# Kernel optimization log

Measured on AMD Instinct MI355X. Metric: run time of the kernel, lower is better.

The kernel has to match this reference:

```python
import jax, jax.numpy as jnp
import numpy as np

D_MODEL = 1024

def setup_inputs() -> dict:
    key = jax.random.key(0)
    kx, kq, kk, kv, ko = jax.random.split(key, 5)
    B, S, D = 8, 2048, D_MODEL
    scale = 1.0 / np.sqrt(D)
    x = jax.random.normal(kx, (B, S, D), dtype=jnp.float32)
    # nn.Linear weights are [out, in]; y = x @ W.T
    Wq = jax.random.normal(kq, (D, D), dtype=jnp.float32) * scale
    Wk = jax.random.normal(kk, (D, D), dtype=jnp.float32) * scale
    Wv = jax.random.normal(kv, (D, D), dtype=jnp.float32) * scale
    Wo = jax.random.normal(ko, (D, D), dtype=jnp.float32) * scale
    return {"x": x, "Wq": Wq, "Wk": Wk, "Wv": Wv, "Wo": Wo}

def reference(x, Wq, Wk, Wv, Wo):
    # Single-head self-attention, dropout in eval mode (identity).
    d_model = x.shape[-1]
    q = jnp.einsum('bsd,ed->bse', x, Wq)
    k = jnp.einsum('bsd,ed->bse', x, Wk)
    v = jnp.einsum('bsd,ed->bse', x, Wv)
    scores = jnp.einsum('bqe,bke->bqk', q, k) / jnp.sqrt(jnp.float32(d_model))
    attn = jax.nn.softmax(scores, axis=-1)
    weighted = jnp.einsum('bqk,bke->bqe', attn, v)
    return jnp.einsum('bqe,oe->bqo', weighted, Wo)
```

## Files before the change

### kernel.cpp

```cpp
#include <hip/hip_runtime.h>
#include <hip/hip_bf16.h>
#include <stdint.h>

typedef short bf16x8 __attribute__((ext_vector_type(8)));
typedef float f32x4 __attribute__((ext_vector_type(4)));

__device__ __forceinline__ unsigned short f2bf(float x) {
  uint32_t u = __builtin_bit_cast(uint32_t, x);
  u += 0x7FFFu + ((u >> 16) & 1u);
  return (unsigned short)(u >> 16);
}
__device__ __forceinline__ float bf2f(unsigned short u) {
  uint32_t v = ((uint32_t)u) << 16;
  return __builtin_bit_cast(float, v);
}

__device__ __forceinline__ void gl2lds16(const void* g, void* l) {
  __builtin_amdgcn_global_load_lds(
      (const __attribute__((address_space(1))) unsigned int*)g,
      (__attribute__((address_space(3))) unsigned int*)l, 16, 0, 0);
}

__global__ __launch_bounds__(256) void cast_f32_bf16_k(
    const float* __restrict__ s, unsigned short* __restrict__ d, long n) {
  long i = ((long)blockIdx.x * 256 + threadIdx.x) * 8;
  if (i >= n) return;
  float4 a = *(const float4*)(s + i);
  float4 b = *(const float4*)(s + i + 4);
  bf16x8 o;
  o[0] = (short)f2bf(a.x); o[1] = (short)f2bf(a.y);
  o[2] = (short)f2bf(a.z); o[3] = (short)f2bf(a.w);
  o[4] = (short)f2bf(b.x); o[5] = (short)f2bf(b.y);
  o[6] = (short)f2bf(b.z); o[7] = (short)f2bf(b.w);
  *(bf16x8*)(d + i) = o;
}

__global__ __launch_bounds__(256) void cast4_f32_bf16_k(
    const float* __restrict__ s0, const float* __restrict__ s1,
    const float* __restrict__ s2, const float* __restrict__ s3,
    unsigned short* __restrict__ d, long n) {
  const float* s = blockIdx.z == 0 ? s0 : blockIdx.z == 1 ? s1 : blockIdx.z == 2 ? s2 : s3;
  long i = ((long)blockIdx.x * 256 + threadIdx.x) * 8;
  if (i >= n) return;
  float4 a = *(const float4*)(s + i);
  float4 b = *(const float4*)(s + i + 4);
  bf16x8 o;
  o[0] = (short)f2bf(a.x); o[1] = (short)f2bf(a.y);
  o[2] = (short)f2bf(a.z); o[3] = (short)f2bf(a.w);
  o[4] = (short)f2bf(b.x); o[5] = (short)f2bf(b.y);
  o[6] = (short)f2bf(b.z); o[7] = (short)f2bf(b.w);
  *(bf16x8*)(d + blockIdx.z * n + i) = o;
}

template <typename OutT, bool FUSEQKV>
__global__ __launch_bounds__(512, 2) void gemm_bt8(
    const unsigned short* __restrict__ A, const unsigned short* __restrict__ B,
    OutT* __restrict__ C, int M, int N, int K,
    long sA, long sB, long sC, float alpha) {
  extern __shared__ __align__(16) char smem[];
  const int bz = blockIdx.z;
  const int gx = gridDim.x;
  const int nwg = gx * gridDim.y;
  const int idx = blockIdx.y * gx + blockIdx.x;
  const int wg = (idx & 7) * (nwg >> 3) + (idx >> 3);
  const int bm = wg / gx, bn = wg % gx;

  const int tid = threadIdx.x, lane = tid & 63, wave = tid >> 6;
  const int wm = wave >> 2, wn = wave & 3;

  const char* Ac = (const char*)(A + (long)bz * sA + (long)bm * 256 * K);
  const char* Bc = (const char*)(B + (long)bz * sB + (long)bn * 256 * K);
  C += (long)bz * sC;
  const long ld = (long)K * 2;

  const int sr8 = tid >> 3;
  const int scolx = (((tid & 7) ^ ((tid >> 3) & 7)) << 4);

  auto stageHalf = [&](int t, int op, int h, const char* gbase) {
    char* reg = smem + (((((t & 1) << 1) | op) << 1 | h) << 14);
    const long ktb = (long)t << 7;
#pragma unroll
    for (int c = 0; c < 2; ++c)
      gl2lds16(gbase + (long)(h * 128 + c * 64 + sr8) * ld + ktb + scolx,
               reg + c * 8192 + tid * 16);
  };

  const char* Areg[2] = { smem + ((0 << 2 | wm) << 14),
                          smem + ((1 << 2 | wm) << 14) };
  const char* Breg[2] = { smem + (((0 << 2) | 2 | (wn >> 1)) << 14),
                          smem + (((1 << 2) | 2 | (wn >> 1)) << 14) };
  const int cko[2] = { (((lane >> 4) << 4) ^ ((lane & 7) << 4)),
                       ((64 | ((lane >> 4) << 4)) ^ ((lane & 7) << 4)) };
  const int rowA0 = (lane & 15) * 128;
  const int rowB0 = ((wn & 1) * 64 + (lane & 15)) * 128;

  f32x4 acc[8][4] = {};

  stageHalf(0, 1, 0, Bc); stageHalf(0, 1, 1, Bc);
  stageHalf(0, 0, 0, Ac); stageHalf(0, 0, 1, Ac);
  stageHalf(1, 1, 0, Bc); stageHalf(1, 1, 1, Bc);
  asm volatile("s_waitcnt vmcnt(4)" ::: "memory");
  __builtin_amdgcn_s_barrier();

  const int nt = K >> 6;
  const int niter = nt >> 1;
  for (int i = 0; i < niter; ++i) {
    const int u = 2 * i;
    const bool pf = (i + 1 < niter);
#pragma unroll
    for (int d = 0; d < 2; ++d) {
      bf16x8 b[4][2];
#pragma unroll
      for (int mq = 0; mq < 4; ++mq) {
        bf16x8 a[2][2];
        if (mq == 0) {
#pragma unroll
          for (int n = 0; n < 4; ++n)
#pragma unroll
            for (int kh = 0; kh < 2; ++kh)
              b[n][kh] = *(const bf16x8*)(Breg[d] + rowB0 + n * 2048 + cko[kh]);
        }
#pragma unroll
        for (int j = 0; j < 2; ++j)
#pragma unroll
          for (int kh = 0; kh < 2; ++kh)
            a[j][kh] = *(const bf16x8*)(Areg[d] + rowA0 + (mq * 2 + j) * 2048 + cko[kh]);
        if (d == 0 && mq == 0) { stageHalf(u + 1, 0, 0, Ac); stageHalf(u + 1, 0, 1, Ac); }
        if (d == 0 && mq == 1 && pf) stageHalf(u + 2, 1, 0, Bc);
        if (d == 0 && mq == 2 && pf) stageHalf(u + 2, 1, 1, Bc);
        if (d == 1 && mq == 0 && pf) { stageHalf(u + 2, 0, 0, Ac); stageHalf(u + 2, 0, 1, Ac); }
        if (d == 1 && mq == 1 && pf) stageHalf(u + 3, 1, 0, Bc);
        if (d == 1 && mq == 2 && pf) stageHalf(u + 3, 1, 1, Bc);
        if (mq == 0) asm volatile("s_waitcnt lgkmcnt(8)" ::: "memory");
        __builtin_amdgcn_s_barrier();
        asm volatile("s_waitcnt lgkmcnt(0)" ::: "memory");
        __builtin_amdgcn_sched_barrier(0);
        __builtin_amdgcn_s_setprio(1);
#pragma unroll
        for (int kh = 0; kh < 2; ++kh)
#pragma unroll
          for (int j = 0; j < 2; ++j)
#pragma unroll
            for (int n = 0; n < 4; ++n)
              acc[mq * 2 + j][n] = __builtin_amdgcn_mfma_f32_16x16x32_bf16(
                  a[j][kh], b[n][kh], acc[mq * 2 + j][n], 0, 0, 0);
        __builtin_amdgcn_s_setprio(0);
        if (d == 0 && mq == 3) {
          if (pf) asm volatile("s_waitcnt vmcnt(4)" ::: "memory");
          else    asm volatile("s_waitcnt vmcnt(0)" ::: "memory");
        }
        if (d == 1 && mq == 3 && pf) asm volatile("s_waitcnt vmcnt(4)" ::: "memory");
        __builtin_amdgcn_s_barrier();
      }
    }
  }

  const long row0 = (long)bm * 256 + wm * 128 + (lane >> 4) * 4;
  const int col0 = bn * 256 + wn * 64 + (lane & 15);
  if constexpr (FUSEQKV) {
    const int tensor = bn >> 2;
    unsigned short* dst = (unsigned short*)C + ((long)tensor << 24);
    const int colb0 = col0 - (tensor << 10);
#pragma unroll
    for (int m = 0; m < 8; ++m) {
#pragma unroll
      for (int n = 0; n < 4; ++n) {
        if (tensor < 2) {
#pragma unroll
          for (int r = 0; r < 4; ++r)
            dst[(row0 + m * 16 + r) * 1024 + colb0 + n * 16] = f2bf(acc[m][n][r]);
        } else {
          long row = row0 + m * 16;
          long base = ((row >> 11) << 21) + ((long)(colb0 + n * 16) << 11) + (row & 2047);
          ushort4 st;
          st.x = f2bf(acc[m][n][0]); st.y = f2bf(acc[m][n][1]);
          st.z = f2bf(acc[m][n][2]); st.w = f2bf(acc[m][n][3]);
          *(ushort4*)(dst + base) = st;
        }
      }
    }
  } else {
#pragma unroll
    for (int m = 0; m < 8; ++m) {
#pragma unroll
      for (int n = 0; n < 4; ++n) {
#pragma unroll
        for (int r = 0; r < 4; ++r) {
          long row = row0 + m * 16 + r;
          int col = col0 + n * 16;
          float v = acc[m][n][r] * alpha;
          if constexpr (sizeof(OutT) == 2)
            C[row * (long)N + col] = (OutT)f2bf(v);
          else
            C[row * (long)N + col] = v;
        }
      }
    }
  }
}

__global__ __launch_bounds__(256) void softmax_inplace(unsigned short* __restrict__ s, int C) {
  __shared__ float red[8];
  long row = blockIdx.x;
  unsigned short* p = s + row * (long)C;
  int tid = threadIdx.x, lane = tid & 63, w = tid >> 6;
  bf16x8 raw = *(const bf16x8*)(p + tid * 8);
  float v[8];
  float mx = -3.4e38f;
#pragma unroll
  for (int j = 0; j < 8; ++j) { v[j] = bf2f((unsigned short)raw[j]); mx = fmaxf(mx, v[j]); }
#pragma unroll
  for (int o = 32; o > 0; o >>= 1) mx = fmaxf(mx, __shfl_xor(mx, o));
  if (lane == 0) red[w] = mx;
  __syncthreads();
  mx = fmaxf(fmaxf(red[0], red[1]), fmaxf(red[2], red[3]));
  float sum = 0.f;
#pragma unroll
  for (int j = 0; j < 8; ++j) { v[j] = __expf(v[j] - mx); sum += v[j]; }
#pragma unroll
  for (int o = 32; o > 0; o >>= 1) sum += __shfl_xor(sum, o);
  if (lane == 0) red[4 + w] = sum;
  __syncthreads();
  float inv = 1.f / (red[4] + red[5] + red[6] + red[7]);
  bf16x8 o8;
#pragma unroll
  for (int j = 0; j < 8; ++j) o8[j] = (short)f2bf(v[j] * inv);
  *(bf16x8*)(p + tid * 8) = o8;
}

extern "C" void kernel_launch(void* const* d_in, const int* in_sizes, int n_in,
                              void* d_out, int out_size, void* d_ws, size_t ws_size,
                              hipStream_t stream) {
  (void)in_sizes; (void)n_in; (void)out_size; (void)ws_size;
  const float* x  = (const float*)d_in[0];
  const float* Wq = (const float*)d_in[1];
  const float* Wk = (const float*)d_in[2];
  const float* Wv = (const float*)d_in[3];
  const float* Wo = (const float*)d_in[4];
  const int B = 8, S = 2048, D = 1024;
  const long MB = 1 << 20;
  char* w = (char*)d_ws;
  unsigned short* Wqb = (unsigned short*)(w + 0 * MB);
  unsigned short* Wob = (unsigned short*)(w + 6 * MB);
  unsigned short* xb  = (unsigned short*)(w + 8 * MB);
  unsigned short* qb  = (unsigned short*)(w + 40 * MB);
  unsigned short* kb  = (unsigned short*)(w + 72 * MB);
  unsigned short* vt  = (unsigned short*)(w + 104 * MB);
  unsigned short* wb  = xb;
  unsigned short* attn = (unsigned short*)d_out;
  float* out = (float*)d_out;

  long nx = (long)B * S * D;
  long nw = (long)D * D;

  const int LDSB = 131072;
  hipFuncSetAttribute((const void*)gemm_bt8<unsigned short, true>,
                      hipFuncAttributeMaxDynamicSharedMemorySize, LDSB);
  hipFuncSetAttribute((const void*)gemm_bt8<unsigned short, false>,
                      hipFuncAttributeMaxDynamicSharedMemorySize, LDSB);
  hipFuncSetAttribute((const void*)gemm_bt8<float, false>,
                      hipFuncAttributeMaxDynamicSharedMemorySize, LDSB);

  cast_f32_bf16_k<<<(int)(nx / 2048), 256, 0, stream>>>(x, xb, nx);
  dim3 gW((int)(nw / 2048), 1, 4);
  cast4_f32_bf16_k<<<gW, 256, 0, stream>>>(Wq, Wk, Wv, Wo, Wqb, nw);

  dim3 gF(3072 / 256, (B * S) / 256, 1);
  gemm_bt8<unsigned short, true><<<gF, 512, LDSB, stream>>>(
      xb, Wqb, qb, B * S, 3072, D, 0, 0, 0, 1.f);

  dim3 gS(S / 256, S / 256, B);
  gemm_bt8<unsigned short, false><<<gS, 512, LDSB, stream>>>(qb, kb, attn, S, S, D,
      (long)S * D, (long)S * D, (long)S * S, 0.03125f);

  softmax_inplace<<<B * S, 256, 0, stream>>>(attn, S);

  dim3 gPV(D / 256, S / 256, B);
  gemm_bt8<unsigned short, false><<<gPV, 512, LDSB, stream>>>(attn, vt, wb, S, D, S,
      (long)S * S, (long)D * S, (long)S * D, 1.f);

  dim3 gP(D / 256, (B * S) / 256, 1);
  gemm_bt8<float, false><<<gP, 512, LDSB, stream>>>(wb, Wob, out, B * S, D, D, 0, 0, 0, 1.f);
}
```

Before: 329.4 us.

## Swap GEMM operands so every epilogue writes transposed vectorized stores

The GEMM kernel is generalized with separate leading dimensions for A, B and the output, and it always writes the output transposed, packing four contiguous rows per store. Each matmul is re-expressed with its operands swapped, computing C^T = B·A^T, so the accumulator's four consecutive rows become contiguous in memory. The fused QKV launch is split into three separate GEMMs, and V is written directly in its transposed layout. The aim is to replace scalar 2-byte and 4-byte scattered epilogue stores with 8-byte and 16-byte vector stores, at the cost of losing the single fused QKV launch.

```diff
diff --git a/kernel.cpp b/kernel.cpp
--- a/kernel.cpp
+++ b/kernel.cpp
@@ -52,11 +52,11 @@
   *(bf16x8*)(d + blockIdx.z * n + i) = o;
 }
 
-template <typename OutT, bool FUSEQKV>
-__global__ __launch_bounds__(512, 2) void gemm_bt8(
+template <typename OutT>
+__global__ __launch_bounds__(512, 2) void gemm_tt(
     const unsigned short* __restrict__ A, const unsigned short* __restrict__ B,
-    OutT* __restrict__ C, int M, int N, int K,
-    long sA, long sB, long sC, float alpha) {
+    OutT* __restrict__ C, int K,
+    long sA, long sB, long sC, int ldA, int ldB, int ldT, float alpha) {
   extern __shared__ __align__(16) char smem[];
   const int bz = blockIdx.z;
   const int gx = gridDim.x;
@@ -68,20 +68,20 @@
   const int tid = threadIdx.x, lane = tid & 63, wave = tid >> 6;
   const int wm = wave >> 2, wn = wave & 3;
 
-  const char* Ac = (const char*)(A + (long)bz * sA + (long)bm * 256 * K);
-  const char* Bc = (const char*)(B + (long)bz * sB + (long)bn * 256 * K);
+  const long ldAb = (long)ldA * 2, ldBb = (long)ldB * 2;
+  const char* Ac = (const char*)(A + (long)bz * sA) + (long)bm * 256 * ldAb;
+  const char* Bc = (const char*)(B + (long)bz * sB) + (long)bn * 256 * ldBb;
   C += (long)bz * sC;
-  const long ld = (long)K * 2;
 
   const int sr8 = tid >> 3;
   const int scolx = (((tid & 7) ^ ((tid >> 3) & 7)) << 4);
 
-  auto stageHalf = [&](int t, int op, int h, const char* gbase) {
+  auto stageHalf = [&](int t, int op, int h, const char* gbase, long ldb_) {
     char* reg = smem + (((((t & 1) << 1) | op) << 1 | h) << 14);
     const long ktb = (long)t << 7;
 #pragma unroll
     for (int c = 0; c < 2; ++c)
-      gl2lds16(gbase + (long)(h * 128 + c * 64 + sr8) * ld + ktb + scolx,
+      gl2lds16(gbase + (long)(h * 128 + c * 64 + sr8) * ldb_ + ktb + scolx,
                reg + c * 8192 + tid * 16);
   };
 
@@ -96,9 +96,9 @@
 
   f32x4 acc[8][4] = {};
 
-  stageHalf(0, 1, 0, Bc); stageHalf(0, 1, 1, Bc);
-  stageHalf(0, 0, 0, Ac); stageHalf(0, 0, 1, Ac);
-  stageHalf(1, 1, 0, Bc); stageHalf(1, 1, 1, Bc);
+  stageHalf(0, 1, 0, Bc, ldBb); stageHalf(0, 1, 1, Bc, ldBb);
+  stageHalf(0, 0, 0, Ac, ldAb); stageHalf(0, 0, 1, Ac, ldAb);
+  stageHalf(1, 1, 0, Bc, ldBb); stageHalf(1, 1, 1, Bc, ldBb);
   asm volatile("s_waitcnt vmcnt(4)" ::: "memory");
   __builtin_amdgcn_s_barrier();
 
@@ -125,12 +125,12 @@
 #pragma unroll
           for (int kh = 0; kh < 2; ++kh)
             a[j][kh] = *(const bf16x8*)(Areg[d] + rowA0 + (mq * 2 + j) * 2048 + cko[kh]);
-        if (d == 0 && mq == 0) { stageHalf(u + 1, 0, 0, Ac); stageHalf(u + 1, 0, 1, Ac); }
-        if (d == 0 && mq == 1 && pf) stageHalf(u + 2, 1, 0, Bc);
-        if (d == 0 && mq == 2 && pf) stageHalf(u + 2, 1, 1, Bc);
-        if (d == 1 && mq == 0 && pf) { stageHalf(u + 2, 0, 0, Ac); stageHalf(u + 2, 0, 1, Ac); }
-        if (d == 1 && mq == 1 && pf) stageHalf(u + 3, 1, 0, Bc);
-        if (d == 1 && mq == 2 && pf) stageHalf(u + 3, 1, 1, Bc);
+        if (d == 0 && mq == 0) { stageHalf(u + 1, 0, 0, Ac, ldAb); stageHalf(u + 1, 0, 1, Ac, ldAb); }
+        if (d == 0 && mq == 1 && pf) stageHalf(u + 2, 1, 0, Bc, ldBb);
+        if (d == 0 && mq == 2 && pf) stageHalf(u + 2, 1, 1, Bc, ldBb);
+        if (d == 1 && mq == 0 && pf) { stageHalf(u + 2, 0, 0, Ac, ldAb); stageHalf(u + 2, 0, 1, Ac, ldAb); }
+        if (d == 1 && mq == 1 && pf) stageHalf(u + 3, 1, 0, Bc, ldBb);
+        if (d == 1 && mq == 2 && pf) stageHalf(u + 3, 1, 1, Bc, ldBb);
         if (mq == 0) asm volatile("s_waitcnt lgkmcnt(8)" ::: "memory");
         __builtin_amdgcn_s_barrier();
         asm volatile("s_waitcnt lgkmcnt(0)" ::: "memory");
@@ -157,43 +157,23 @@
 
   const long row0 = (long)bm * 256 + wm * 128 + (lane >> 4) * 4;
   const int col0 = bn * 256 + wn * 64 + (lane & 15);
-  if constexpr (FUSEQKV) {
-    const int tensor = bn >> 2;
-    unsigned short* dst = (unsigned short*)C + ((long)tensor << 24);
-    const int colb0 = col0 - (tensor << 10);
-#pragma unroll
-    for (int m = 0; m < 8; ++m) {
-#pragma unroll
-      for (int n = 0; n < 4; ++n) {
-        if (tensor < 2) {
-#pragma unroll
-          for (int r = 0; r < 4; ++r)
-            dst[(row0 + m * 16 + r) * 1024 + colb0 + n * 16] = f2bf(acc[m][n][r]);
-        } else {
-          long row = row0 + m * 16;
-          long base = ((row >> 11) << 21) + ((long)(colb0 + n * 16) << 11) + (row & 2047);
-          ushort4 st;
-          st.x = f2bf(acc[m][n][0]); st.y = f2bf(acc[m][n][1]);
-          st.z = f2bf(acc[m][n][2]); st.w = f2bf(acc[m][n][3]);
-          *(ushort4*)(dst + base) = st;
-        }
-      }
-    }
-  } else {
-#pragma unroll
-    for (int m = 0; m < 8; ++m) {
-#pragma unroll
-      for (int n = 0; n < 4; ++n) {
-#pragma unroll
-        for (int r = 0; r < 4; ++r) {
-          long row = row0 + m * 16 + r;
-          int col = col0 + n * 16;
-          float v = acc[m][n][r] * alpha;
-          if constexpr (sizeof(OutT) == 2)
-            C[row * (long)N + col] = (OutT)f2bf(v);
-          else
-            C[row * (long)N + col] = v;
-        }
+#pragma unroll
+  for (int m = 0; m < 8; ++m) {
+#pragma unroll
+    for (int n = 0; n < 4; ++n) {
+      long row = row0 + m * 16;
+      long col = col0 + n * 16;
+      long base = col * (long)ldT + row;
+      if constexpr (sizeof(OutT) == 2) {
+        ushort4 st;
+        st.x = f2bf(acc[m][n][0] * alpha); st.y = f2bf(acc[m][n][1] * alpha);
+        st.z = f2bf(acc[m][n][2] * alpha); st.w = f2bf(acc[m][n][3] * alpha);
+        *(ushort4*)((unsigned short*)C + base) = st;
+      } else {
+        float4 st;
+        st.x = acc[m][n][0] * alpha; st.y = acc[m][n][1] * alpha;
+        st.z = acc[m][n][2] * alpha; st.w = acc[m][n][3] * alpha;
+        *(float4*)((float*)C + base) = st;
       }
     }
   }
@@ -241,6 +221,8 @@
   const long MB = 1 << 20;
   char* w = (char*)d_ws;
   unsigned short* Wqb = (unsigned short*)(w + 0 * MB);
+  unsigned short* Wkb = (unsigned short*)(w + 2 * MB);
+  unsigned short* Wvb = (unsigned short*)(w + 4 * MB);
   unsigned short* Wob = (unsigned short*)(w + 6 * MB);
   unsigned short* xb  = (unsigned short*)(w + 8 * MB);
   unsigned short* qb  = (unsigned short*)(w + 40 * MB);
@@ -254,31 +236,35 @@
   long nw = (long)D * D;
 
   const int LDSB = 131072;
-  hipFuncSetAttribute((const void*)gemm_bt8<unsigned short, true>,
+  hipFuncSetAttribute((const void*)gemm_tt<unsigned short>,
                       hipFuncAttributeMaxDynamicSharedMemorySize, LDSB);
-  hipFuncSetAttribute((const void*)gemm_bt8<unsigned short, false>,
-                      hipFuncAttributeMaxDynamicSharedMemorySize, LDSB);
-  hipFuncSetAttribute((const void*)gemm_bt8<float, false>,
+  hipFuncSetAttribute((const void*)gemm_tt<float>,
                       hipFuncAttributeMaxDynamicSharedMemorySize, LDSB);
 
   cast_f32_bf16_k<<<(int)(nx / 2048), 256, 0, stream>>>(x, xb, nx);
   dim3 gW((int)(nw / 2048), 1, 4);
   cast4_f32_bf16_k<<<gW, 256, 0, stream>>>(Wq, Wk, Wv, Wo, Wqb, nw);
 
-  dim3 gF(3072 / 256, (B * S) / 256, 1);
-  gemm_bt8<unsigned short, true><<<gF, 512, LDSB, stream>>>(
-      xb, Wqb, qb, B * S, 3072, D, 0, 0, 0, 1.f);
-
-  dim3 gS(S / 256, S / 256, B);
-  gemm_bt8<unsigned short, false><<<gS, 512, LDSB, stream>>>(qb, kb, attn, S, S, D,
-      (long)S * D, (long)S * D, (long)S * S, 0.03125f);
+  dim3 gQ(64, 4, 1);
+  gemm_tt<unsigned short><<<gQ, 512, LDSB, stream>>>(
+      Wqb, xb, qb, D, 0, 0, 0, D, D, D, 1.f);
+  gemm_tt<unsigned short><<<gQ, 512, LDSB, stream>>>(
+      Wkb, xb, kb, D, 0, 0, 0, D, D, D, 1.f);
+  dim3 gV(4, 64, 1);
+  gemm_tt<unsigned short><<<gV, 512, LDSB, stream>>>(
+      xb, Wvb, vt, D, 0, 0, 0, D, D, B * S, 1.f);
+
+  dim3 gS(8, 8, B);
+  gemm_tt<unsigned short><<<gS, 512, LDSB, stream>>>(
+      kb, qb, attn, D, (long)S * D, (long)S * D, (long)S * S, D, D, S, 0.03125f);
 
   softmax_inplace<<<B * S, 256, 0, stream>>>(attn, S);
 
-  dim3 gPV(D / 256, S / 256, B);
-  gemm_bt8<unsigned short, false><<<gPV, 512, LDSB, stream>>>(attn, vt, wb, S, D, S,
-      (long)S * S, (long)D * S, (long)S * D, 1.f);
-
-  dim3 gP(D / 256, (B * S) / 256, 1);
-  gemm_bt8<float, false><<<gP, 512, LDSB, stream>>>(wb, Wob, out, B * S, D, D, 0, 0, 0, 1.f);
-}
+  dim3 gPV(8, 4, B);
+  gemm_tt<unsigned short><<<gPV, 512, LDSB, stream>>>(
+      vt, attn, wb, S, (long)S, (long)S * S, (long)S * D, B * S, S, D, 1.f);
+
+  dim3 gO(64, 4, 1);
+  gemm_tt<float><<<gO, 512, LDSB, stream>>>(
+      Wob, wb, out, D, 0, 0, 0, D, D, D, 1.f);
+}
```

Measured after the change: 343.8 us. 1.04x slower.
